# Kernel tuning notes

Measured on AMD Instinct MI355X. Metric: run time of the kernel, lower is better.

## Reference

```python
import jax, jax.numpy as jnp
import numpy as np

VIN, VOUT, E, H = 32000, 32000, 1024, 1024
TS, TT, B = 50, 48, 64


def _lstm_scan(x, m, Wih, Whh, bih, bhh):
    """Masked (packed-sequence-equivalent) LSTM. x:(T,B,E), m:(T,B) bool valid."""
    Bn, Hn = x.shape[1], Whh.shape[1]

    def step(carry, tm):
        h, c = carry
        xt, mt = tm
        gates = xt @ Wih.T + bih + h @ Whh.T + bhh
        i, f, g, o = jnp.split(gates, 4, axis=-1)  # torch gate order i,f,g,o
        c_new = jax.nn.sigmoid(f) * c + jax.nn.sigmoid(i) * jnp.tanh(g)
        h_new = jax.nn.sigmoid(o) * jnp.tanh(c_new)
        mt_ = mt[:, None]
        return (jnp.where(mt_, h_new, h), jnp.where(mt_, c_new, c)), jnp.where(mt_, h_new, 0.0)

    init = (jnp.zeros((Bn, Hn), x.dtype), jnp.zeros((Bn, Hn), x.dtype))
    (h, c), outs = jax.lax.scan(step, init, (x, m))
    return outs, h, c


def setup_inputs() -> dict:
    key = jax.random.key(0)
    ks = jax.random.split(key, 32)
    s = 0.02
    src = jax.random.randint(ks[0], (TS, B), 0, VIN)
    src_len = jnp.sort(jax.random.randint(ks[1], (B,), TS // 2, TS + 1))[::-1]
    src_len = src_len.at[0].set(TS)  # pad_packed pads to max length in batch
    trg = jax.random.randint(ks[2], (TT, B), 0, VOUT)
    p = lambda k, shp: jax.random.normal(k, shp, jnp.float32) * s
    return {
        "src": src, "src_len": src_len, "trg": trg,
        "enc_emb": p(ks[3], (VIN, E)),
        "Wih_f": p(ks[4], (4 * H, E)), "Whh_f": p(ks[5], (4 * H, H)),
        "bih_f": p(ks[6], (4 * H,)), "bhh_f": p(ks[7], (4 * H,)),
        "Wih_b": p(ks[8], (4 * H, E)), "Whh_b": p(ks[9], (4 * H, H)),
        "bih_b": p(ks[10], (4 * H,)), "bhh_b": p(ks[11], (4 * H,)),
        "Wfch": p(ks[12], (H, 2 * H)), "bfch": p(ks[13], (H,)),
        "Wfcc": p(ks[14], (H, 2 * H)), "bfcc": p(ks[15], (H,)),
        "dec_emb": p(ks[16], (VOUT, H)),
        "Wih_d": p(ks[17], (4 * H, 2 * H)), "Whh_d": p(ks[18], (4 * H, H)),
        "bih_d": p(ks[19], (4 * H,)), "bhh_d": p(ks[20], (4 * H,)),
        "Wattn": p(ks[21], (H, 2 * H)), "battn": p(ks[22], (H,)),
        "Wcomb": p(ks[23], (H, 3 * H)), "bcomb": p(ks[24], (H,)),
        "Wout": p(ks[25], (VOUT, H)), "bout": p(ks[26], (VOUT,)),
    }


def reference(src, src_len, trg, enc_emb, Wih_f, Whh_f, bih_f, bhh_f,
              Wih_b, Whh_b, bih_b, bhh_b, Wfch, bfch, Wfcc, bfcc, dec_emb,
              Wih_d, Whh_d, bih_d, bhh_d, Wattn, battn, Wcomb, bcomb, Wout, bout):
    T, Bn = src.shape
    emb = enc_emb[src]                                      # (T,B,E)
    m = jnp.arange(T)[:, None] < src_len[None, :]           # (T,B) valid
    outs_f, hf, cf = _lstm_scan(emb, m, Wih_f, Whh_f, bih_f, bhh_f)
    outs_b, hb, cb = _lstm_scan(emb[::-1], m[::-1], Wih_b, Whh_b, bih_b, bhh_b)
    outs_b = outs_b[::-1]
    enc_outputs = jnp.concatenate([outs_f, outs_b], -1).transpose(1, 0, 2)  # (B,T,2H)
    hidden = jnp.concatenate([hf, hb], -1) @ Wfch.T + bfch  # (B,H)
    cell = jnp.concatenate([cf, cb], -1) @ Wfcc.T + bfcc
    mask_pad = ~m.T                                          # (B,T) True at pads

    attn_proj = jnp.einsum('btd,hd->bth', enc_outputs, Wattn) + battn  # (B,T,H)
    dec_emb_seq = dec_emb[trg]                               # (TT,B,H), dropout=eval

    def dstep(carry, emb_t):
        h, c, dout = carry
        x = jnp.concatenate([emb_t, dout], -1)               # (B, H+H)
        gates = x @ Wih_d.T + bih_d + h @ Whh_d.T + bhh_d
        i, f, g, o = jnp.split(gates, 4, axis=-1)
        c_new = jax.nn.sigmoid(f) * c + jax.nn.sigmoid(i) * jnp.tanh(g)
        h_new = jax.nn.sigmoid(o) * jnp.tanh(c_new)
        scores = jnp.einsum('bth,bh->bt', attn_proj, h_new)
        scores = jnp.where(mask_pad, -jnp.inf, scores)
        w = jax.nn.softmax(scores, -1)
        ctx = jnp.einsum('bt,btd->bd', w, enc_outputs)       # (B,2H)
        dout_new = jnp.concatenate([ctx, h_new], -1) @ Wcomb.T + bcomb
        logits = jax.nn.relu(dout_new) @ Wout.T + bout       # (B,VOUT)
        return (h_new, c_new, dout_new), logits

    init = (hidden, cell, jnp.zeros_like(hidden))
    _, logits = jax.lax.scan(dstep, init, dec_emb_seq[:-1])  # (TT-1,B,V)
    return logits.transpose(1, 2, 0)                         # (B,V,TT-1)
```

## Files before the change

### kernel.cpp

```cpp
#include <hip/hip_runtime.h>
#include <hip/hip_bf16.h>
#include <math.h>


typedef __attribute__((ext_vector_type(8))) short short8;
typedef __attribute__((ext_vector_type(4))) float floatx4;
typedef unsigned short u16;

#define DEV static __device__ __forceinline__

DEV float bf2f(u16 u){ union{unsigned int i; float f;} v; v.i = ((unsigned int)u)<<16; return v.f; }
DEV u16 f2bf(float f){
  union{float f; unsigned int i;} v; v.f = f;
  unsigned int i = v.i;
  return (u16)((i + 0x7fffu + ((i>>16)&1u)) >> 16);
}
DEV float sigm(float x){ return 1.f/(1.f+expf(-x)); }

__global__ __launch_bounds__(256) void cvt2d(const float* __restrict__ src, long sld,
                                             u16* __restrict__ dst, long dld, long cols)
{
  long r = blockIdx.x;
  long c = ((long)blockIdx.y*256 + threadIdx.x)*4;
  if (c >= cols) return;
  const float4 v = *(const float4*)(src + r*sld + c);
  u16* d = dst + r*dld + c;
  d[0]=f2bf(v.x); d[1]=f2bf(v.y); d[2]=f2bf(v.z); d[3]=f2bf(v.w);
}

DEV void split_store(const float4 v, u16* d, u16* e){
  u16 h0=f2bf(v.x), h1=f2bf(v.y), h2=f2bf(v.z), h3=f2bf(v.w);
  d[0]=h0; d[1]=h1; d[2]=h2; d[3]=h3;
  e[0]=f2bf(v.x-bf2f(h0)); e[1]=f2bf(v.y-bf2f(h1));
  e[2]=f2bf(v.z-bf2f(h2)); e[3]=f2bf(v.w-bf2f(h3));
}

__global__ __launch_bounds__(256) void cvtA(
    const float* s0, const float* s1, const float* s2, const float* s3,
    u16* h0, u16* h1, u16* h2, u16* h3,
    u16* l0, u16* l1, u16* l2, u16* l3)
{
  const float* s; u16* h; u16* l;
  switch (blockIdx.z){
    case 0: s=s0; h=h0; l=l0; break;
    case 1: s=s1; h=h1; l=l1; break;
    case 2: s=s2; h=h2; l=l2; break;
    default: s=s3; h=h3; l=l3; break;
  }
  long r = blockIdx.x; long c = (long)threadIdx.x*4;
  split_store(*(const float4*)(s + r*1024 + c), h + r*1024 + c, l + r*1024 + c);
}

__global__ __launch_bounds__(256) void cvtB(
    const float* s0, long sld0, const float* s1, long sld1,
    const float* s2, long sld2, const float* s3, long sld3,
    u16* h0, u16* h1, u16* h2, u16* h3,
    u16* l0, u16* l1, u16* l2, u16* l3)
{
  const float* s; u16* h; u16* l; long sld;
  switch (blockIdx.z){
    case 0: s=s0; h=h0; l=l0; sld=sld0; break;
    case 1: s=s1; h=h1; l=l1; sld=sld1; break;
    case 2: s=s2; h=h2; l=l2; sld=sld2; break;
    default: s=s3; h=h3; l=l3; sld=sld3; break;
  }
  long r = blockIdx.x;
  long c = ((long)blockIdx.y*256 + threadIdx.x)*4;
  split_store(*(const float4*)(s + r*sld + c), h + r*2048 + c, l + r*2048 + c);
}

__global__ __launch_bounds__(256) void cvtC(
    const float* s0, long sld0, u16* h0, u16* l0, long dld0,
    const float* s1, long sld1, u16* h1, u16* l1, long dld1,
    const float* s2, long sld2, u16* h2, u16* l2, long dld2)
{
  const float* s; u16* h; u16* l; long sld, dld;
  switch (blockIdx.z){
    case 0: s=s0; h=h0; l=l0; sld=sld0; dld=dld0; break;
    case 1: s=s1; h=h1; l=l1; sld=sld1; dld=dld1; break;
    default: s=s2; h=h2; l=l2; sld=sld2; dld=dld2; break;
  }
  long r = blockIdx.x; long c = (long)threadIdx.x*4;
  split_store(*(const float4*)(s + r*sld + c), h + r*dld + c, l + r*dld + c);
}

__global__ __launch_bounds__(256) void cvt_cell_split(const float* __restrict__ c_all,
                                                      u16* __restrict__ hi, u16* __restrict__ lo)
{
  int b = blockIdx.x, tid = threadIdx.x;
  for (int k = 0; k < 8; k++){
    int u = tid + k*256;
    int dir = u >> 10, uu = u & 1023;
    float v = c_all[dir*65536 + b*1024 + uu];
    u16 h = f2bf(v);
    hi[b*2048 + u] = h;
    lo[b*2048 + u] = f2bf(v - bf2f(h));
  }
}

__global__ __launch_bounds__(256) void bias_combine(
    const float* a1,const float* a2,float* o1,
    const float* b1,const float* b2,float* o2,
    const float* c1,const float* c2,float* o3,
    const float* battn, float* o4)
{
  int i = blockIdx.x*256 + threadIdx.x;
  if (i < 4096){ o1[i]=a1[i]+a2[i]; o2[i]=b1[i]+b2[i]; o3[i]=c1[i]+c2[i]; }
  if (i < 2048) o4[i] = (i < 1024) ? battn[i] : 0.f;
}

__global__ __launch_bounds__(256) void zero_u32(unsigned int* p, int n){
  int i = blockIdx.x*256 + threadIdx.x;
  if (i < n) p[i] = 0;
}

__global__ __launch_bounds__(256) void gather_embed_split(const int* __restrict__ idx,
                                                          const float* __restrict__ tab,
                                                          u16* __restrict__ hi, u16* __restrict__ lo)
{
  int r = blockIdx.x, tid = threadIdx.x;
  int tok = idx[r];
  float4 v = ((const float4*)(tab + (long)tok*1024))[tid];
  split_store(v, hi + (long)r*1024 + tid*4, lo + (long)r*1024 + tid*4);
}

template<int AS, int BS>
__global__ __launch_bounds__(256) void gemm128(
    const u16* __restrict__ Ahi, const u16* __restrict__ Alo, int lda,
    const u16* __restrict__ Bhi, const u16* __restrict__ Blo, int ldb,
    int M, int N, int K,
    const float* __restrict__ bias,
    float* __restrict__ Cf, int ldc)
{
  __shared__ u16 Ash[128][36];
  __shared__ u16 Bsh[128][36];
  __shared__ u16 Asl[AS?128:1][36];
  __shared__ u16 Bsl[BS?128:1][36];
  const int tid = threadIdx.x;
  const int lane = tid & 63;
  const int w = tid >> 6, wm = w >> 1, wn = w & 1;
  const int m0 = blockIdx.x * 128;
  const int n0 = blockIdx.y * 128;

  floatx4 acc[4][4];
  #pragma unroll
  for (int i=0;i<4;i++)
    #pragma unroll
    for (int j=0;j<4;j++) acc[i][j] = (floatx4)0.f;

  const int seg = tid & 3;
  const int rowh = tid >> 2;
  const int nk = K >> 5;
  for (int kk = 0; kk < nk; kk++) {
    int kbase = kk*32 + seg*8;
    #pragma unroll
    for (int p=0;p<2;p++){
      int r = rowh + p*64;
      bool okA = (m0 + r < M);
      int4 va = okA ? *(const int4*)(Ahi + (long)(m0+r)*lda + kbase) : make_int4(0,0,0,0);
      *(int4*)&Ash[r][seg*8] = va;
      if (AS){
        int4 vl = okA ? *(const int4*)(Alo + (long)(m0+r)*lda + kbase) : make_int4(0,0,0,0);
        *(int4*)&Asl[r][seg*8] = vl;
      }
      *(int4*)&Bsh[r][seg*8] = *(const int4*)(Bhi + (long)(n0+r)*ldb + kbase);
      if (BS)
        *(int4*)&Bsl[r][seg*8] = *(const int4*)(Blo + (long)(n0+r)*ldb + kbase);
    }
    __syncthreads();
    short8 ah[4], bh[4], al[4], bl[4];
    #pragma unroll
    for (int i=0;i<4;i++){
      ah[i] = *(const short8*)&Ash[wm*64 + i*16 + (lane&15)][(lane>>4)*8];
      if (AS) al[i] = *(const short8*)&Asl[wm*64 + i*16 + (lane&15)][(lane>>4)*8];
    }
    #pragma unroll
    for (int j=0;j<4;j++){
      bh[j] = *(const short8*)&Bsh[wn*64 + j*16 + (lane&15)][(lane>>4)*8];
      if (BS) bl[j] = *(const short8*)&Bsl[wn*64 + j*16 + (lane&15)][(lane>>4)*8];
    }
    #pragma unroll
    for (int i=0;i<4;i++)
      #pragma unroll
      for (int j=0;j<4;j++){
        acc[i][j] = __builtin_amdgcn_mfma_f32_16x16x32_bf16(ah[i], bh[j], acc[i][j], 0,0,0);
        if (AS) acc[i][j] = __builtin_amdgcn_mfma_f32_16x16x32_bf16(al[i], bh[j], acc[i][j], 0,0,0);
        if (BS) acc[i][j] = __builtin_amdgcn_mfma_f32_16x16x32_bf16(ah[i], bl[j], acc[i][j], 0,0,0);
      }
    __syncthreads();
  }
  const int rb0 = (lane>>4)*4, cf = lane & 15;
  #pragma unroll
  for (int i=0;i<4;i++){
    #pragma unroll
    for (int j=0;j<4;j++){
      int n = n0 + wn*64 + j*16 + cf;
      #pragma unroll
      for (int r=0;r<4;r++){
        int m = m0 + wm*64 + i*16 + rb0 + r;
        if (m >= M) continue;
        Cf[(long)m*ldc + n] = acc[i][j][r] + (bias ? bias[n] : 0.f);
      }
    }
  }
}

template<int MODE>
__global__ __launch_bounds__(256) void gemm64(
    const u16* __restrict__ Ahi, const u16* __restrict__ Alo, int lda,
    const u16* __restrict__ Bhi, const u16* __restrict__ Blo, int ldb,
    int K, const float* __restrict__ bias,
    float* __restrict__ outF,
    u16* __restrict__ o1hi, u16* __restrict__ o1lo)
{
  __shared__ u16 Ash[64][36], Asl[64][36];
  __shared__ u16 Bsh[64][36], Bsl[64][36];
  const int tid = threadIdx.x, lane = tid&63, w = tid>>6;
  const int n0 = blockIdx.x * 64;
  floatx4 acc[4];
  #pragma unroll
  for (int i=0;i<4;i++) acc[i]=(floatx4)0.f;
  const int seg = tid&3, row = tid>>2;
  const int nk = K>>5;
  for (int kk=0; kk<nk; kk++){
    int kbase = kk*32 + seg*8;
    *(int4*)&Ash[row][seg*8] = *(const int4*)(Ahi + (long)row*lda + kbase);
    *(int4*)&Asl[row][seg*8] = *(const int4*)(Alo + (long)row*lda + kbase);
    *(int4*)&Bsh[row][seg*8] = *(const int4*)(Bhi + (long)(n0+row)*ldb + kbase);
    *(int4*)&Bsl[row][seg*8] = *(const int4*)(Blo + (long)(n0+row)*ldb + kbase);
    __syncthreads();
    short8 bh = *(const short8*)&Bsh[w*16 + (lane&15)][(lane>>4)*8];
    short8 bl = *(const short8*)&Bsl[w*16 + (lane&15)][(lane>>4)*8];
    #pragma unroll
    for (int i=0;i<4;i++){
      short8 ah = *(const short8*)&Ash[i*16 + (lane&15)][(lane>>4)*8];
      short8 al = *(const short8*)&Asl[i*16 + (lane&15)][(lane>>4)*8];
      acc[i] = __builtin_amdgcn_mfma_f32_16x16x32_bf16(ah, bh, acc[i], 0,0,0);
      acc[i] = __builtin_amdgcn_mfma_f32_16x16x32_bf16(al, bh, acc[i], 0,0,0);
      acc[i] = __builtin_amdgcn_mfma_f32_16x16x32_bf16(ah, bl, acc[i], 0,0,0);
    }
    __syncthreads();
  }
  const int rb0 = (lane>>4)*4, cf = lane&15;
  int n = n0 + w*16 + cf;
  #pragma unroll
  for (int i=0;i<4;i++){
    #pragma unroll
    for (int r=0;r<4;r++){
      int m = i*16 + rb0 + r;
      float v = acc[i][r] + bias[n];
      if (MODE == 0){
        u16 h = f2bf(v), l = f2bf(v - bf2f(h));
        o1hi[m*2048 + n] = h; o1lo[m*2048 + n] = l;
      } else {
        outF[m*1024 + n] = v;
      }
    }
  }
}

__global__ __launch_bounds__(256) void enc_step(
    int s,
    const u16* __restrict__ hin_hi, const u16* __restrict__ hin_lo,
    u16* __restrict__ hout_hi, u16* __restrict__ hout_lo,
    float* __restrict__ c_all,
    const u16* __restrict__ Whhf_hi, const u16* __restrict__ Whhf_lo,
    const u16* __restrict__ Whhb_hi, const u16* __restrict__ Whhb_lo,
    const float* __restrict__ Gfb,
    const float* __restrict__ bias_f, const float* __restrict__ bias_b,
    const int* __restrict__ src_len,
    u16* __restrict__ eo_hi, u16* __restrict__ eo_lo)
{
  __shared__ u16 Ah[32][1032], Al[32][1032];
  __shared__ float gl[4][32][17];
  const int tid = threadIdx.x, lane = tid&63, w = tid>>6;
  const int dir = blockIdx.x >> 7;
  const int r7 = blockIdx.x & 127;
  const int u0 = (r7 >> 1) * 16;
  const int b0 = (r7 & 1) * 32;
  const u16* Whh_hi = dir ? Whhb_hi : Whhf_hi;
  const u16* Whh_lo = dir ? Whhb_lo : Whhf_lo;
  const float* bias = dir ? bias_b : bias_f;
  const int trow = dir ? (49 - s) : s;

  {
    int row = tid>>3, c0 = (tid&7)*8;
    const u16* sh = hin_hi + dir*1024 + (b0+row)*2048;
    const u16* sl = hin_lo + dir*1024 + (b0+row)*2048;
    #pragma unroll
    for (int j=0;j<16;j++){
      int c = c0 + j*64;
      *(int4*)&Ah[row][c] = *(const int4*)(sh + c);
      *(int4*)&Al[row][c] = *(const int4*)(sl + c);
    }
  }
  __syncthreads();

  const int rowb = w*1024 + u0 + (lane&15);
  const int cseg = (lane>>4)*8;
  const u16* bhp = Whh_hi + (long)rowb*1024 + cseg;
  const u16* blp = Whh_lo + (long)rowb*1024 + cseg;
  floatx4 acc0 = (floatx4)0.f, acc1 = (floatx4)0.f;
  #pragma unroll 4
  for (int kk=0; kk<32; kk++){
    int kbase = kk*32;
    short8 bh = *(const short8*)(bhp + kbase);
    short8 bl = *(const short8*)(blp + kbase);
    short8 ah0 = *(const short8*)&Ah[lane&15][kbase + cseg];
    short8 al0 = *(const short8*)&Al[lane&15][kbase + cseg];
    short8 ah1 = *(const short8*)&Ah[16 + (lane&15)][kbase + cseg];
    short8 al1 = *(const short8*)&Al[16 + (lane&15)][kbase + cseg];
    acc0 = __builtin_amdgcn_mfma_f32_16x16x32_bf16(ah0, bh, acc0, 0,0,0);
    acc0 = __builtin_amdgcn_mfma_f32_16x16x32_bf16(al0, bh, acc0, 0,0,0);
    acc0 = __builtin_amdgcn_mfma_f32_16x16x32_bf16(ah0, bl, acc0, 0,0,0);
    acc1 = __builtin_amdgcn_mfma_f32_16x16x32_bf16(ah1, bh, acc1, 0,0,0);
    acc1 = __builtin_amdgcn_mfma_f32_16x16x32_bf16(al1, bh, acc1, 0,0,0);
    acc1 = __builtin_amdgcn_mfma_f32_16x16x32_bf16(ah1, bl, acc1, 0,0,0);
  }
  __syncthreads();
  const int rb0 = (lane>>4)*4, cf = lane&15;
  #pragma unroll
  for (int r=0;r<4;r++){
    gl[w][rb0 + r][cf]      = acc0[r];
    gl[w][16 + rb0 + r][cf] = acc1[r];
  }
  __syncthreads();
  for (int k=0;k<2;k++){
    int idx = tid + k*256;
    int bl_ = idx >> 4, u = idx & 15;
    int b = b0 + bl_, uu = u0 + u;
    long grow = (long)(trow*64 + b)*8192 + dir*4096;
    float gi = gl[0][bl_][u] + Gfb[grow +        uu] + bias[uu];
    float gf = gl[1][bl_][u] + Gfb[grow + 1024 + uu] + bias[1024+uu];
    float gg2 = gl[2][bl_][u] + Gfb[grow + 2048 + uu] + bias[2048+uu];
    float go = gl[3][bl_][u] + Gfb[grow + 3072 + uu] + bias[3072+uu];
    float c_old = c_all[dir*65536 + b*1024 + uu];
    float c_new = sigm(gf)*c_old + sigm(gi)*tanhf(gg2);
    float h_new = sigm(go)*tanhf(c_new);
    bool valid = trow < src_len[b];
    if (valid) c_all[dir*65536 + b*1024 + uu] = c_new;
    u16 hh = f2bf(h_new);
    u16 hl = f2bf(h_new - bf2f(hh));
    int hidx = b*2048 + dir*1024 + uu;
    hout_hi[hidx] = valid ? hh : hin_hi[hidx];
    hout_lo[hidx] = valid ? hl : hin_lo[hidx];
    long eidx = (long)(b*50 + trow)*2048 + dir*1024 + uu;
    eo_hi[eidx] = valid ? hh : (u16)0;
    eo_lo[eidx] = valid ? hl : (u16)0;
  }
}

__global__ __launch_bounds__(256) void dec_gates(
    int t,
    const u16* __restrict__ ain_hi, const u16* __restrict__ ain_lo,
    u16* __restrict__ aout_hi, u16* __restrict__ aout_lo,
    float* __restrict__ c_dec,
    const u16* __restrict__ Wcat_hi, const u16* __restrict__ Wcat_lo,
    const float* __restrict__ Gd,
    const float* __restrict__ bias_d,
    float* __restrict__ hf32)
{
  __shared__ u16 Ah[16][2056], Al[16][2056];
  __shared__ float gl[4][16][17];
  const int tid=threadIdx.x, lane=tid&63, w=tid>>6;
  const int u0 = (blockIdx.x >> 2) * 16;
  const int b0 = (blockIdx.x & 3) * 16;

  {
    int row = tid>>4, c0 = (tid&15)*8;
    const u16* sh = ain_hi + (b0+row)*2048;
    const u16* sl = ain_lo + (b0+row)*2048;
    #pragma unroll
    for (int j=0;j<16;j++){
      int c = c0 + j*128;
      *(int4*)&Ah[row][c] = *(const int4*)(sh + c);
      *(int4*)&Al[row][c] = *(const int4*)(sl + c);
    }
  }
  __syncthreads();

  const int rowb = w*1024 + u0 + (lane&15);
  const int cseg = (lane>>4)*8;
  const u16* bhp = Wcat_hi + (long)rowb*2048 + cseg;
  const u16* blp = Wcat_lo + (long)rowb*2048 + cseg;
  floatx4 acc = (floatx4)0.f;
  #pragma unroll 4
  for (int kk=0; kk<64; kk++){
    int kbase = kk*32;
    short8 bh = *(const short8*)(bhp + kbase);
    short8 bl = *(const short8*)(blp + kbase);
    short8 ah = *(const short8*)&Ah[lane&15][kbase + cseg];
    short8 al = *(const short8*)&Al[lane&15][kbase + cseg];
    acc = __builtin_amdgcn_mfma_f32_16x16x32_bf16(ah,bh,acc,0,0,0);
    acc = __builtin_amdgcn_mfma_f32_16x16x32_bf16(al,bh,acc,0,0,0);
    acc = __builtin_amdgcn_mfma_f32_16x16x32_bf16(ah,bl,acc,0,0,0);
  }
  __syncthreads();
  const int rb0=(lane>>4)*4, cf=lane&15;
  #pragma unroll
  for(int r=0;r<4;r++) gl[w][rb0+r][cf] = acc[r];
  __syncthreads();
  {
    int bl_ = tid>>4, u = tid&15;
    int b = b0 + bl_, uu = u0 + u;
    long grow = (long)(t*64 + b)*4096;
    float gi = gl[0][bl_][u] + Gd[grow +        uu] + bias_d[uu];
    float gf = gl[1][bl_][u] + Gd[grow + 1024 + uu] + bias_d[1024+uu];
    float gg2 = gl[2][bl_][u] + Gd[grow + 2048 + uu] + bias_d[2048+uu];
    float go = gl[3][bl_][u] + Gd[grow + 3072 + uu] + bias_d[3072+uu];
    float c_old = c_dec[b*1024+uu];
    float c_new = sigm(gf)*c_old + sigm(gi)*tanhf(gg2);
    float h_new = sigm(go)*tanhf(c_new);
    c_dec[b*1024+uu] = c_new;
    u16 hh = f2bf(h_new);
    u16 hl = f2bf(h_new - bf2f(hh));
    aout_hi[b*2048 + uu] = hh;  aout_lo[b*2048 + uu] = hl;
    hf32[b*1024 + uu] = h_new;
  }
}

__global__ __launch_bounds__(256) void attn_w(
    const float* __restrict__ APf,
    const float* __restrict__ hf32,
    const int* __restrict__ src_len,
    float* __restrict__ wout)
{
  __shared__ float h_sh[1024];
  __shared__ float sc_sh[50];
  const int tid = threadIdx.x, lane = tid&63, w = tid>>6;
  const int b = blockIdx.x;
  for (int i = tid; i < 1024; i += 256) h_sh[i] = hf32[b*1024 + i];
  __syncthreads();
  for (int tp = w; tp < 50; tp += 4){
    const float* ap = APf + (long)(b*50+tp)*2048;
    float p = 0.f;
    #pragma unroll
    for (int i=0;i<16;i++){ int d = lane + i*64; p += ap[d]*h_sh[d]; }
    #pragma unroll
    for (int off=32; off>0; off>>=1) p += __shfl_down(p, off);
    if (lane==0) sc_sh[tp] = p;
  }
  __syncthreads();
  if (w == 0){
    int len = src_len[b];
    float s = (lane < 50 && lane < len) ? sc_sh[lane] : -3.4e38f;
    float mx = s;
    #pragma unroll
    for (int off=32; off>0; off>>=1) mx = fmaxf(mx, __shfl_xor(mx, off));
    float p = (lane < 50 && lane < len) ? expf(s - mx) : 0.f;
    float sum = p;
    #pragma unroll
    for (int off=32; off>0; off>>=1) sum += __shfl_xor(sum, off);
    if (lane < 50) wout[b*50 + lane] = p / sum;
  }
}

__global__ __launch_bounds__(256) void dout_step(
    int t,
    const u16* __restrict__ h_hi, const u16* __restrict__ h_lo,
    const u16* __restrict__ Wch_h, const u16* __restrict__ Wch_l,
    const float* __restrict__ APf,
    const float* __restrict__ wout,
    const float* __restrict__ bcomb,
    u16* __restrict__ ac_hi, u16* __restrict__ ac_lo,
    u16* __restrict__ dall_h, u16* __restrict__ dall_l)
{
  __shared__ u16 Ash[4][16][36], Asl[4][16][36];
  __shared__ u16 Bsh[4][16][36], Bsl[4][16][36];
  __shared__ float gl[4][16][17];
  const int tid=threadIdx.x, lane=tid&63, w=tid>>6;
  const int n0 = (blockIdx.x >> 2) * 16;
  const int b0 = (blockIdx.x & 3) * 16;
  floatx4 acc = (floatx4)0.f;
  const int r = lane&15, sg = lane>>4;
  for (int kk=0; kk<8; kk++){
    int kb = w*256 + kk*32 + sg*8;
    *(int4*)&Ash[w][r][sg*8] = *(const int4*)(h_hi + (b0+r)*2048 + kb);
    *(int4*)&Asl[w][r][sg*8] = *(const int4*)(h_lo + (b0+r)*2048 + kb);
    *(int4*)&Bsh[w][r][sg*8] = *(const int4*)(Wch_h + (long)(n0+r)*1024 + kb);
    *(int4*)&Bsl[w][r][sg*8] = *(const int4*)(Wch_l + (long)(n0+r)*1024 + kb);
    __syncthreads();
    short8 ah = *(const short8*)&Ash[w][lane&15][(lane>>4)*8];
    short8 al = *(const short8*)&Asl[w][lane&15][(lane>>4)*8];
    short8 bh = *(const short8*)&Bsh[w][lane&15][(lane>>4)*8];
    short8 bl = *(const short8*)&Bsl[w][lane&15][(lane>>4)*8];
    acc = __builtin_amdgcn_mfma_f32_16x16x32_bf16(ah,bh,acc,0,0,0);
    acc = __builtin_amdgcn_mfma_f32_16x16x32_bf16(al,bh,acc,0,0,0);
    acc = __builtin_amdgcn_mfma_f32_16x16x32_bf16(ah,bl,acc,0,0,0);
    __syncthreads();
  }
  const int rb0=(lane>>4)*4, cf=lane&15;
  #pragma unroll
  for(int rr=0;rr<4;rr++) gl[w][rb0+rr][cf] = acc[rr];
  __syncthreads();
  {
    int bl_ = tid>>4, nl = tid&15;
    int b = b0 + bl_, nn = n0 + nl;
    float v = gl[0][bl_][nl]+gl[1][bl_][nl]+gl[2][bl_][nl]+gl[3][bl_][nl] + bcomb[nn];
    const float* wp = wout + b*50;
    const float* Pp = APf + (long)(b*50)*2048 + 1024 + nn;
    for (int tp=0; tp<50; tp++) v += wp[tp] * Pp[(long)tp*2048];
    u16 h = f2bf(v), l = f2bf(v - bf2f(h));
    ac_hi[b*2048 + 1024 + nn] = h;  ac_lo[b*2048 + 1024 + nn] = l;
    float rv = v > 0.f ? v : 0.f;
    u16 rh = f2bf(rv), rl = f2bf(rv - bf2f(rh));
    long o = (long)(b*47 + t)*1024 + nn;
    dall_h[o] = rh;  dall_l[o] = rl;
  }
}

__global__ __launch_bounds__(256) void logits_gemm(
    const u16* __restrict__ Wout_bf,
    const u16* __restrict__ dall_h, const u16* __restrict__ dall_l,
    const float* __restrict__ bout,
    float* __restrict__ out)
{
  __shared__ u16 Wsh[256][36];
  __shared__ u16 Dh[48][36], Dl[48][36];
  const int tid = threadIdx.x, lane = tid&63, w = tid>>6;
  const int b = blockIdx.x;
  const int v0 = blockIdx.y * 256;
  floatx4 acc[4][3];
  #pragma unroll
  for (int i=0;i<4;i++)
    #pragma unroll
    for (int j=0;j<3;j++) acc[i][j]=(floatx4)0.f;
  const int lrow = tid>>1, lseg = tid&1;
  for (int kk=0; kk<32; kk++){
    int kb = kk*32;
    #pragma unroll
    for (int p=0;p<2;p++){
      int row = lrow + p*128;
      const u16* src = Wout_bf + (long)(v0+row)*1024 + kb + lseg*16;
      *(int4*)&Wsh[row][lseg*16]     = *(const int4*)(src);
      *(int4*)&Wsh[row][lseg*16 + 8] = *(const int4*)(src + 8);
    }
    if (tid < 96){
      int row = tid>>1, sg = tid&1;
      long a = (long)(b*47+row)*1024 + kb + sg*16;
      *(int4*)&Dh[row][sg*16]     = *(const int4*)(dall_h + a);
      *(int4*)&Dh[row][sg*16 + 8] = *(const int4*)(dall_h + a + 8);
      *(int4*)&Dl[row][sg*16]     = *(const int4*)(dall_l + a);
      *(int4*)&Dl[row][sg*16 + 8] = *(const int4*)(dall_l + a + 8);
    }
    __syncthreads();
    short8 av[4];
    #pragma unroll
    for (int i=0;i<4;i++)
      av[i] = *(const short8*)&Wsh[w*64 + i*16 + (lane&15)][(lane>>4)*8];
    #pragma unroll
    for (int j=0;j<3;j++){
      short8 bh = *(const short8*)&Dh[j*16 + (lane&15)][(lane>>4)*8];
      short8 bl = *(const short8*)&Dl[j*16 + (lane&15)][(lane>>4)*8];
      #pragma unroll
      for (int i=0;i<4;i++){
        acc[i][j] = __builtin_amdgcn_mfma_f32_16x16x32_bf16(av[i], bh, acc[i][j], 0,0,0);
        acc[i][j] = __builtin_amdgcn_mfma_f32_16x16x32_bf16(av[i], bl, acc[i][j], 0,0,0);
      }
    }
    __syncthreads();
  }
  const int rb0=(lane>>4)*4, cf=lane&15;
  #pragma unroll
  for (int i=0;i<4;i++){
    #pragma unroll
    for (int j=0;j<3;j++){
      int tt = j*16 + cf;
      if (tt >= 47) continue;
      #pragma unroll
      for (int r=0;r<4;r++){
        int v = v0 + w*64 + i*16 + rb0 + r;
        out[(long)b*1504000 + (long)v*47 + tt] = acc[i][j][r] + bout[v];
      }
    }
  }
}

extern "C" void kernel_launch(void* const* d_in, const int* in_sizes, int n_in,
                              void* d_out, int out_size, void* d_ws, size_t ws_size,
                              hipStream_t stream)
{
  (void)in_sizes; (void)n_in; (void)out_size; (void)ws_size;
  const int*   src     = (const int*)d_in[0];
  const int*   src_len = (const int*)d_in[1];
  const int*   trg     = (const int*)d_in[2];
  const float* enc_emb = (const float*)d_in[3];
  const float* Wih_f   = (const float*)d_in[4];
  const float* Whh_f   = (const float*)d_in[5];
  const float* bih_f   = (const float*)d_in[6];
  const float* bhh_f   = (const float*)d_in[7];
  const float* Wih_b   = (const float*)d_in[8];
  const float* Whh_b   = (const float*)d_in[9];
  const float* bih_b   = (const float*)d_in[10];
  const float* bhh_b   = (const float*)d_in[11];
  const float* Wfch    = (const float*)d_in[12];
  const float* bfch    = (const float*)d_in[13];
  const float* Wfcc    = (const float*)d_in[14];
  const float* bfcc    = (const float*)d_in[15];
  const float* dec_emb = (const float*)d_in[16];
  const float* Wih_d   = (const float*)d_in[17];
  const float* Whh_d   = (const float*)d_in[18];
  const float* bih_d   = (const float*)d_in[19];
  const float* bhh_d   = (const float*)d_in[20];
  const float* Wattn   = (const float*)d_in[21];
  const float* battn   = (const float*)d_in[22];
  const float* Wcomb   = (const float*)d_in[23];
  const float* bcomb   = (const float*)d_in[24];
  const float* Wout    = (const float*)d_in[25];
  const float* bout    = (const float*)d_in[26];
  float* out = (float*)d_out;

  size_t off = 0;
  auto alloc = [&](size_t bytes)->void*{
    void* p = (char*)d_ws + off; off += (bytes + 255) & ~(size_t)255; return p; };

  u16* Wenc_h = (u16*)alloc((size_t)8192*1024*2);  u16* Wenc_l = (u16*)alloc((size_t)8192*1024*2);
  u16* Whhf_h = (u16*)alloc((size_t)4096*1024*2);  u16* Whhf_l = (u16*)alloc((size_t)4096*1024*2);
  u16* Whhb_h = (u16*)alloc((size_t)4096*1024*2);  u16* Whhb_l = (u16*)alloc((size_t)4096*1024*2);
  u16* WihdA_h= (u16*)alloc((size_t)4096*1024*2);  u16* WihdA_l= (u16*)alloc((size_t)4096*1024*2);
  u16* Wcat_h = (u16*)alloc((size_t)4096*2048*2);  u16* Wcat_l = (u16*)alloc((size_t)4096*2048*2);
  u16* Wfch_h = (u16*)alloc((size_t)1024*2048*2);  u16* Wfch_l = (u16*)alloc((size_t)1024*2048*2);
  u16* Wfcc_h = (u16*)alloc((size_t)1024*2048*2);  u16* Wfcc_l = (u16*)alloc((size_t)1024*2048*2);
  u16* Wap_h  = (u16*)alloc((size_t)2048*2048*2);  u16* Wap_l  = (u16*)alloc((size_t)2048*2048*2);
  u16* Wch_h  = (u16*)alloc((size_t)1024*1024*2);  u16* Wch_l  = (u16*)alloc((size_t)1024*1024*2);
  u16* Wout_bf =(u16*)alloc((size_t)32000*1024*2);
  u16* embx_h = (u16*)alloc((size_t)3200*1024*2);  u16* embx_l = (u16*)alloc((size_t)3200*1024*2);
  u16* dembx_h= (u16*)alloc((size_t)3008*1024*2);  u16* dembx_l= (u16*)alloc((size_t)3008*1024*2);
  float* Gfb  = (float*)alloc((size_t)3200*8192*4);
  float* Gd   = (float*)alloc((size_t)3008*4096*4);
  u16* eo_h  = (u16*)alloc((size_t)3200*2048*2);
  u16* eo_l  = (u16*)alloc((size_t)3200*2048*2);
  u16* h0_h  = (u16*)alloc((size_t)64*2048*2);  u16* h0_l  = (u16*)alloc((size_t)64*2048*2);
  u16* h1_h  = (u16*)alloc((size_t)64*2048*2);  u16* h1_l  = (u16*)alloc((size_t)64*2048*2);
  u16* cfin_h= (u16*)alloc((size_t)64*2048*2);  u16* cfin_l= (u16*)alloc((size_t)64*2048*2);
  u16* ac0_h = (u16*)alloc((size_t)64*2048*2);  u16* ac0_l = (u16*)alloc((size_t)64*2048*2);
  u16* ac1_h = (u16*)alloc((size_t)64*2048*2);  u16* ac1_l = (u16*)alloc((size_t)64*2048*2);
  u16* dall_h= (u16*)alloc((size_t)3009*1024*2); u16* dall_l= (u16*)alloc((size_t)3009*1024*2);
  float* APf   = (float*)alloc((size_t)3200*2048*4);
  float* c_enc = (float*)alloc((size_t)2*64*1024*4);
  float* c_dec = (float*)alloc((size_t)64*1024*4);
  float* hf32  = (float*)alloc((size_t)64*1024*4);
  float* wout  = (float*)alloc((size_t)64*50*4);
  float* bias_f = (float*)alloc(4096*4);
  float* bias_b = (float*)alloc(4096*4);
  float* bias_d = (float*)alloc(4096*4);
  float* bias_ap= (float*)alloc(2048*4);

  cvtA<<<dim3(4096,1,4),256,0,stream>>>(Wih_f, Wih_b, Whh_f, Whh_b,
                                        Wenc_h, Wenc_h + (size_t)4096*1024, Whhf_h, Whhb_h,
                                        Wenc_l, Wenc_l + (size_t)4096*1024, Whhf_l, Whhb_l);
  cvtB<<<dim3(1024,2,4),256,0,stream>>>(Wfch, 2048, Wfcc, 2048, Wattn, 2048, Wcomb, 3072,
                                        Wfch_h, Wfcc_h, Wap_h, Wap_h + (size_t)1024*2048,
                                        Wfch_l, Wfcc_l, Wap_l, Wap_l + (size_t)1024*2048);
  cvtC<<<dim3(4096,1,3),256,0,stream>>>(Wih_d, 2048, WihdA_h, WihdA_l, 1024,
                                        Whh_d, 1024, Wcat_h, Wcat_l, 2048,
                                        Wih_d + 1024, 2048, Wcat_h + 1024, Wcat_l + 1024, 2048);
  cvtC<<<dim3(1024,1,1),256,0,stream>>>(Wcomb + 2048, 3072, Wch_h, Wch_l, 1024,
                                        Wcomb + 2048, 3072, Wch_h, Wch_l, 1024,
                                        Wcomb + 2048, 3072, Wch_h, Wch_l, 1024);
  cvt2d<<<dim3(32000,1),256,0,stream>>>(Wout, 1024, Wout_bf, 1024, 1024);
  bias_combine<<<16,256,0,stream>>>(bih_f,bhh_f,bias_f, bih_b,bhh_b,bias_b, bih_d,bhh_d,bias_d, battn,bias_ap);

  gather_embed_split<<<3200,256,0,stream>>>(src, enc_emb, embx_h, embx_l);
  gather_embed_split<<<3008,256,0,stream>>>(trg, dec_emb, dembx_h, dembx_l);

  zero_u32<<<256,256,0,stream>>>((unsigned int*)h0_h, 65536);
  zero_u32<<<256,256,0,stream>>>((unsigned int*)h0_l, 65536);
  zero_u32<<<256,256,0,stream>>>((unsigned int*)ac0_h, 65536);
  zero_u32<<<256,256,0,stream>>>((unsigned int*)ac0_l, 65536);
  zero_u32<<<512,256,0,stream>>>((unsigned int*)c_enc, 131072);

  gemm128<1,1><<<dim3(25,64),256,0,stream>>>(embx_h, embx_l, 1024, Wenc_h, Wenc_l, 1024, 3200, 8192, 1024, nullptr, Gfb, 8192);
  gemm128<1,1><<<dim3(24,32),256,0,stream>>>(dembx_h, dembx_l, 1024, WihdA_h, WihdA_l, 1024, 3008, 4096, 1024, nullptr, Gd, 4096);

  u16* hh_[2] = {h0_h, h1_h};
  u16* hl_[2] = {h0_l, h1_l};
  for (int s=0; s<50; s++)
    enc_step<<<256,256,0,stream>>>(s, hh_[s&1], hl_[s&1], hh_[(s+1)&1], hl_[(s+1)&1], c_enc,
                                   Whhf_h, Whhf_l, Whhb_h, Whhb_l, Gfb, bias_f, bias_b, src_len, eo_h, eo_l);

  cvt_cell_split<<<64,256,0,stream>>>(c_enc, cfin_h, cfin_l);

  gemm128<1,1><<<dim3(25,16),256,0,stream>>>(eo_h, eo_l, 2048, Wap_h, Wap_l, 2048, 3200, 2048, 2048, bias_ap, APf, 2048);

  gemm64<0><<<16,256,0,stream>>>(h0_h, h0_l, 2048, Wfch_h, Wfch_l, 2048, 2048, bfch, nullptr, ac0_h, ac0_l);
  gemm64<1><<<16,256,0,stream>>>(cfin_h, cfin_l, 2048, Wfcc_h, Wfcc_l, 2048, 2048, bfcc, c_dec, nullptr, nullptr);

  u16* ah_[2] = {ac0_h, ac1_h};
  u16* al_[2] = {ac0_l, ac1_l};
  for (int t=0; t<47; t++){
    int cur = t&1, nxt = (t+1)&1;
    dec_gates<<<256,256,0,stream>>>(t, ah_[cur], al_[cur], ah_[nxt], al_[nxt], c_dec,
                                    Wcat_h, Wcat_l, Gd, bias_d, hf32);
    attn_w<<<64,256,0,stream>>>(APf, hf32, src_len, wout);
    dout_step<<<256,256,0,stream>>>(t, ah_[nxt], al_[nxt], Wch_h, Wch_l, APf, wout, bcomb,
                                    ah_[nxt], al_[nxt], dall_h, dall_l);
  }

  logits_gemm<<<dim3(64,125),256,0,stream>>>(Wout_bf, dall_h, dall_l, bout, out);
}
```

Before: 4.847 ms.

## Drop low-bf16 half of decoder outputs and remap block indices for locality

The logits GEMM now uses only the bf16-rounded decoder output instead of a hi/lo split pair, which halves its MFMA count and removes the dall_l buffer and its loads and stores. The logits grid is also rebuilt so that each x-slice covers a contiguous range of vocabulary tiles across all batches, likely so blocks that share Wout rows run together and reuse them in cache. Block-index decoding in enc_step, dec_gates and dout_step is reordered so consecutive blocks share the same batch slice. Dropping the low half lowers the precision of the final projection, which risks tolerance failures. The 8x1024 logits grid launches some blocks that return immediately.

```diff
diff --git a/kernel.cpp b/kernel.cpp
--- a/kernel.cpp
+++ b/kernel.cpp
@@ -274,10 +274,9 @@
   __shared__ u16 Ah[32][1032], Al[32][1032];
   __shared__ float gl[4][32][17];
   const int tid = threadIdx.x, lane = tid&63, w = tid>>6;
-  const int dir = blockIdx.x >> 7;
-  const int r7 = blockIdx.x & 127;
-  const int u0 = (r7 >> 1) * 16;
-  const int b0 = (r7 & 1) * 32;
+  const int b0  = (blockIdx.x >> 7) * 32;
+  const int dir = (blockIdx.x >> 6) & 1;
+  const int u0  = (blockIdx.x & 63) * 16;
   const u16* Whh_hi = dir ? Whhb_hi : Whhf_hi;
   const u16* Whh_lo = dir ? Whhb_lo : Whhf_lo;
   const float* bias = dir ? bias_b : bias_f;
@@ -363,8 +362,8 @@
   __shared__ u16 Ah[16][2056], Al[16][2056];
   __shared__ float gl[4][16][17];
   const int tid=threadIdx.x, lane=tid&63, w=tid>>6;
-  const int u0 = (blockIdx.x >> 2) * 16;
-  const int b0 = (blockIdx.x & 3) * 16;
+  const int b0 = (blockIdx.x >> 6) * 16;
+  const int u0 = (blockIdx.x & 63) * 16;
 
   {
     int row = tid>>4, c0 = (tid&15)*8;
@@ -463,14 +462,14 @@
     const float* __restrict__ wout,
     const float* __restrict__ bcomb,
     u16* __restrict__ ac_hi, u16* __restrict__ ac_lo,
-    u16* __restrict__ dall_h, u16* __restrict__ dall_l)
+    u16* __restrict__ dall_h)
 {
   __shared__ u16 Ash[4][16][36], Asl[4][16][36];
   __shared__ u16 Bsh[4][16][36], Bsl[4][16][36];
   __shared__ float gl[4][16][17];
   const int tid=threadIdx.x, lane=tid&63, w=tid>>6;
-  const int n0 = (blockIdx.x >> 2) * 16;
-  const int b0 = (blockIdx.x & 3) * 16;
+  const int b0 = ((blockIdx.x >> 6) & 3) * 16;
+  const int n0 = (blockIdx.x & 63) * 16;
   floatx4 acc = (floatx4)0.f;
   const int r = lane&15, sg = lane>>4;
   for (int kk=0; kk<8; kk++){
@@ -503,23 +502,27 @@
     u16 h = f2bf(v), l = f2bf(v - bf2f(h));
     ac_hi[b*2048 + 1024 + nn] = h;  ac_lo[b*2048 + 1024 + nn] = l;
     float rv = v > 0.f ? v : 0.f;
-    u16 rh = f2bf(rv), rl = f2bf(rv - bf2f(rh));
-    long o = (long)(b*47 + t)*1024 + nn;
-    dall_h[o] = rh;  dall_l[o] = rl;
+    dall_h[(long)(b*47 + t)*1024 + nn] = f2bf(rv);
   }
 }
 
 __global__ __launch_bounds__(256) void logits_gemm(
     const u16* __restrict__ Wout_bf,
-    const u16* __restrict__ dall_h, const u16* __restrict__ dall_l,
+    const u16* __restrict__ dall_h,
     const float* __restrict__ bout,
     float* __restrict__ out)
 {
+  const int x = blockIdx.x;
+  const int y = blockIdx.y;
+  const int cnt = (x < 5) ? 16 : 15;
+  if (y >= cnt*64) return;
+  const int vt = ((x < 5) ? x*16 : 80 + (x-5)*15) + (y >> 6);
+  const int b  = y & 63;
+  const int v0 = vt * 256;
+
   __shared__ u16 Wsh[256][36];
-  __shared__ u16 Dh[48][36], Dl[48][36];
+  __shared__ u16 Dh[48][36];
   const int tid = threadIdx.x, lane = tid&63, w = tid>>6;
-  const int b = blockIdx.x;
-  const int v0 = blockIdx.y * 256;
   floatx4 acc[4][3];
   #pragma unroll
   for (int i=0;i<4;i++)
@@ -540,8 +543,6 @@
       long a = (long)(b*47+row)*1024 + kb + sg*16;
       *(int4*)&Dh[row][sg*16]     = *(const int4*)(dall_h + a);
       *(int4*)&Dh[row][sg*16 + 8] = *(const int4*)(dall_h + a + 8);
-      *(int4*)&Dl[row][sg*16]     = *(const int4*)(dall_l + a);
-      *(int4*)&Dl[row][sg*16 + 8] = *(const int4*)(dall_l + a + 8);
     }
     __syncthreads();
     short8 av[4];
@@ -551,12 +552,9 @@
     #pragma unroll
     for (int j=0;j<3;j++){
       short8 bh = *(const short8*)&Dh[j*16 + (lane&15)][(lane>>4)*8];
-      short8 bl = *(const short8*)&Dl[j*16 + (lane&15)][(lane>>4)*8];
       #pragma unroll
-      for (int i=0;i<4;i++){
+      for (int i=0;i<4;i++)
         acc[i][j] = __builtin_amdgcn_mfma_f32_16x16x32_bf16(av[i], bh, acc[i][j], 0,0,0);
-        acc[i][j] = __builtin_amdgcn_mfma_f32_16x16x32_bf16(av[i], bl, acc[i][j], 0,0,0);
-      }
     }
     __syncthreads();
   }
@@ -635,7 +633,7 @@
   u16* cfin_h= (u16*)alloc((size_t)64*2048*2);  u16* cfin_l= (u16*)alloc((size_t)64*2048*2);
   u16* ac0_h = (u16*)alloc((size_t)64*2048*2);  u16* ac0_l = (u16*)alloc((size_t)64*2048*2);
   u16* ac1_h = (u16*)alloc((size_t)64*2048*2);  u16* ac1_l = (u16*)alloc((size_t)64*2048*2);
-  u16* dall_h= (u16*)alloc((size_t)3009*1024*2); u16* dall_l= (u16*)alloc((size_t)3009*1024*2);
+  u16* dall_h= (u16*)alloc((size_t)3009*1024*2);
   float* APf   = (float*)alloc((size_t)3200*2048*4);
   float* c_enc = (float*)alloc((size_t)2*64*1024*4);
   float* c_dec = (float*)alloc((size_t)64*1024*4);
@@ -694,8 +692,8 @@
                                     Wcat_h, Wcat_l, Gd, bias_d, hf32);
     attn_w<<<64,256,0,stream>>>(APf, hf32, src_len, wout);
     dout_step<<<256,256,0,stream>>>(t, ah_[nxt], al_[nxt], Wch_h, Wch_l, APf, wout, bcomb,
-                                    ah_[nxt], al_[nxt], dall_h, dall_l);
-  }
-
-  logits_gemm<<<dim3(64,125),256,0,stream>>>(Wout_bf, dall_h, dall_l, bout, out);
-}
+                                    ah_[nxt], al_[nxt], dall_h);
+  }
+
+  logits_gemm<<<dim3(8,1024),256,0,stream>>>(Wout_bf, dall_h, bout, out);
+}
```

Result: faster. 4.550 ms (-6.1%).
